# Kernel tuning notes

Hardware: AMD Instinct MI355X
Metric: run time of the kernel (lower is better)

Reference implementation:

```python
import jax, jax.numpy as jnp
import numpy as np

B, N, C = 4, 2048, 768
H = 12
HD = C // H
SCALE = HD ** -0.5


def setup_inputs() -> dict:
    key = jax.random.key(0)
    k1, k2, k3 = jax.random.split(key, 3)
    x = jax.random.normal(k1, (B, N, C), dtype=jnp.float32)
    w_qkv = jax.random.normal(k2, (3 * C, C), dtype=jnp.float32) * (C ** -0.5)
    w_proj = jax.random.normal(k3, (C, C), dtype=jnp.float32) * (C ** -0.5)
    b_proj = jnp.zeros((C,), dtype=jnp.float32)
    return {"x": x, "w_qkv": w_qkv, "w_proj": w_proj, "b_proj": b_proj}


def reference(x, w_qkv, w_proj, b_proj):
    Bx, Nx, Cx = x.shape
    # qkv linear: x @ W^T -> [B, N, 3C], then split into heads
    qkv = jnp.einsum('bnc,dc->bnd', x, w_qkv)
    qkv = qkv.reshape(Bx, Nx, 3, H, HD).transpose(2, 0, 3, 1, 4)  # [3, B, H, N, HD]
    q, k, v = qkv[0], qkv[1], qkv[2]
    attn = jnp.einsum('bhqd,bhkd->bhqk', q, k) * SCALE  # [B, H, N, N]
    attn = jax.nn.softmax(attn, axis=-1)
    out = jnp.einsum('bhqk,bhkd->bhqd', attn, v)  # [B, H, N, HD]
    out = out.transpose(0, 2, 1, 3).reshape(Bx, Nx, Cx)
    out = jnp.einsum('bnc,dc->bnd', out, w_proj) + b_proj
    return out
```

## Files before the change

### kernel.cpp

```cpp
#include <hip/hip_runtime.h>
#include <hip/hip_bf16.h>
#include <stdint.h>

#define DI __device__ __forceinline__

typedef __bf16 bf16x8 __attribute__((ext_vector_type(8)));
typedef float f32x4 __attribute__((ext_vector_type(4)));
typedef unsigned short u16;

DI u16 f2bf(float f) {
  union { float f; uint32_t u; } x; x.f = f;
  uint32_t r = (x.u + 0x7FFFu + ((x.u >> 16) & 1u)) >> 16;
  return (u16)r;
}
DI bf16x8 load16(const u16* p) { return *(const bf16x8*)p; }

DI void async_copy16(void* lds, const void* g) {
  __builtin_amdgcn_global_load_lds(
      (const __attribute__((address_space(1))) uint32_t*)g,
      (__attribute__((address_space(3))) uint32_t*)lds, 16, 0, 0);
}

DI f32x4 mfma16(bf16x8 a, bf16x8 b, f32x4 c) {
  return __builtin_amdgcn_mfma_f32_16x16x32_bf16(a, b, c, 0, 0, 0);
}

DI float redsum16(float v) {
  v += __shfl_xor(v, 1);
  v += __shfl_xor(v, 2);
  v += __shfl_xor(v, 4);
  v += __shfl_xor(v, 8);
  return v;
}

DI uint32_t pk_bf16(float a, float b) {
  union { __hip_bfloat162 v; uint32_t u; } r;
  r.v = __float22bfloat162_rn(make_float2(a, b));
  return r.u;
}

#define QSCALE (0.125f * 1.44269504088896340736f)

__global__ __launch_bounds__(256)
void cvt_all(const float* __restrict__ s0, u16* __restrict__ d0, int n0,
             const float* __restrict__ s1, u16* __restrict__ d1, int n1,
             const float* __restrict__ s2, u16* __restrict__ d2, int n2) {
  int i = (blockIdx.x * 256 + threadIdx.x) * 4;
  const float* s; u16* d;
  if (i < n0) { s = s0 + i; d = d0 + i; }
  else if (i < n0 + n1) { s = s1 + (i - n0); d = d1 + (i - n0); }
  else if (i < n0 + n1 + n2) { s = s2 + (i - n0 - n1); d = d2 + (i - n0 - n1); }
  else return;
  float4 v = *(const float4*)s;
  ushort4 o;
  o.x = f2bf(v.x); o.y = f2bf(v.y); o.z = f2bf(v.z); o.w = f2bf(v.w);
  *(ushort4*)d = o;
}

__global__ __launch_bounds__(256)
void gemm_qkv(const u16* __restrict__ A, const u16* __restrict__ Bm,
              u16* __restrict__ Qb, u16* __restrict__ Kb, u16* __restrict__ Vt,
              int M, int N, int K) {
  __shared__ u16 As[128 * 32];
  __shared__ u16 Bs[128 * 32];

  const int tid  = threadIdx.x;
  const int lane = tid & 63;
  const int wave = tid >> 6;
  const int m0 = blockIdx.y * 128;
  const int n0 = blockIdx.x * 128;
  const int wm = (wave & 1) * 64;
  const int wn = (wave >> 1) * 64;
  const int c = lane & 15;
  const int g = lane >> 4;

  f32x4 acc[4][4] = {};

  for (int k0 = 0; k0 < K; k0 += 32) {
#pragma unroll
    for (int i = 0; i < 2; ++i) {
      int j = i * 256 + tid;
      int row = j >> 2;
      int col = (j & 3) * 8;
      async_copy16(&As[j * 8], &A[(size_t)(m0 + row) * K + k0 + col]);
      async_copy16(&Bs[j * 8], &Bm[(size_t)(n0 + row) * K + k0 + col]);
    }
    __syncthreads();

    bf16x8 af[4], bfr[4];
#pragma unroll
    for (int t = 0; t < 4; ++t) {
      af[t]  = *(const bf16x8*)&As[(wm + t * 16 + c) * 32 + g * 8];
      bfr[t] = *(const bf16x8*)&Bs[(wn + t * 16 + c) * 32 + g * 8];
    }
#pragma unroll
    for (int mt = 0; mt < 4; ++mt)
#pragma unroll
      for (int nt = 0; nt < 4; ++nt)
        acc[mt][nt] = mfma16(af[mt], bfr[nt], acc[mt][nt]);
    __syncthreads();
  }

  if (n0 < 768) {
#pragma unroll
    for (int nt = 0; nt < 4; ++nt) {
      int col = n0 + wn + nt * 16 + c;
#pragma unroll
      for (int mt = 0; mt < 4; ++mt)
#pragma unroll
        for (int r = 0; r < 4; ++r) {
          int row = m0 + wm + mt * 16 + g * 4 + r;
          Qb[(size_t)row * 768 + col] = f2bf(acc[mt][nt][r] * QSCALE);
        }
    }
  } else if (n0 < 1536) {
#pragma unroll
    for (int nt = 0; nt < 4; ++nt) {
      int col = n0 - 768 + wn + nt * 16 + c;
#pragma unroll
      for (int mt = 0; mt < 4; ++mt)
#pragma unroll
        for (int r = 0; r < 4; ++r) {
          int row = m0 + wm + mt * 16 + g * 4 + r;
          Kb[(size_t)row * 768 + col] = f2bf(acc[mt][nt][r]);
        }
    }
  } else {
#pragma unroll
    for (int nt = 0; nt < 4; ++nt) {
      int cv = n0 - 1536 + wn + nt * 16 + c;
      int hv = cv >> 6, d = cv & 63;
#pragma unroll
      for (int mt = 0; mt < 4; ++mt) {
        int row = m0 + wm + mt * 16 + g * 4;
        int b = row >> 11, nn = row & 2047;
        ushort4 o;
        o.x = f2bf(acc[mt][nt][0]); o.y = f2bf(acc[mt][nt][1]);
        o.z = f2bf(acc[mt][nt][2]); o.w = f2bf(acc[mt][nt][3]);
        *(ushort4*)&Vt[(((size_t)b * 12 + hv) * 64 + d) * 2048 + nn] = o;
      }
    }
  }
}

__global__ __launch_bounds__(256)
void gemm_proj(const u16* __restrict__ A, const u16* __restrict__ Bm,
               const float* __restrict__ bias, float* __restrict__ Co,
               int M, int N, int K) {
  __shared__ u16 As[128 * 32];
  __shared__ u16 Bs[128 * 32];

  const int tid  = threadIdx.x;
  const int lane = tid & 63;
  const int wave = tid >> 6;
  const int m0 = blockIdx.y * 128;
  const int n0 = blockIdx.x * 128;
  const int wm = (wave & 1) * 64;
  const int wn = (wave >> 1) * 64;
  const int c = lane & 15;
  const int g = lane >> 4;

  f32x4 acc[4][4] = {};

  for (int k0 = 0; k0 < K; k0 += 32) {
#pragma unroll
    for (int i = 0; i < 2; ++i) {
      int j = i * 256 + tid;
      int row = j >> 2;
      int col = (j & 3) * 8;
      async_copy16(&As[j * 8], &A[(size_t)(m0 + row) * K + k0 + col]);
      async_copy16(&Bs[j * 8], &Bm[(size_t)(n0 + row) * K + k0 + col]);
    }
    __syncthreads();

    bf16x8 af[4], bfr[4];
#pragma unroll
    for (int t = 0; t < 4; ++t) {
      af[t]  = *(const bf16x8*)&As[(wm + t * 16 + c) * 32 + g * 8];
      bfr[t] = *(const bf16x8*)&Bs[(wn + t * 16 + c) * 32 + g * 8];
    }
#pragma unroll
    for (int mt = 0; mt < 4; ++mt)
#pragma unroll
      for (int nt = 0; nt < 4; ++nt)
        acc[mt][nt] = mfma16(af[mt], bfr[nt], acc[mt][nt]);
    __syncthreads();
  }

#pragma unroll
  for (int nt = 0; nt < 4; ++nt) {
    int col = n0 + wn + nt * 16 + c;
    float bv = bias[col];
#pragma unroll
    for (int mt = 0; mt < 4; ++mt)
#pragma unroll
      for (int r = 0; r < 4; ++r) {
        int row = m0 + wm + mt * 16 + g * 4 + r;
        Co[(size_t)row * N + col] = acc[mt][nt][r] + bv;
      }
  }
}

__global__ __launch_bounds__(256)
void attn_flash(const u16* __restrict__ Qb, const u16* __restrict__ Kb,
                const u16* __restrict__ Vt, u16* __restrict__ out) {
  __shared__ u16 Ks[2 * 64 * 32];
  __shared__ u16 Vs[2 * 64 * 32];
  __shared__ __align__(16) u16 Plds[4][32 * 72];

  const int tid  = threadIdx.x;
  const int lane = tid & 63;
  const int wave = tid >> 6;
  const int idx = blockIdx.x;
  const int qchunk = idx & 15;
  const int h = (idx >> 4) % 12;
  const int b = idx / (16 * 12);
  const int q0 = qchunk * 128 + wave * 32;
  const int c = lane & 15;
  const int g = lane >> 4;

  const u16* Qp = Qb + (size_t)b * 2048 * 768 + h * 64;
  const u16* Kp = Kb + (size_t)b * 2048 * 768 + h * 64;
  const u16* Vp = Vt + ((size_t)b * 12 + h) * 64 * 2048;

  u16* pw = &Plds[wave][0];

  const bf16x8 qf0 = load16(&Qp[(size_t)(q0 + c) * 768 + g * 8]);
  const bf16x8 qf1 = load16(&Qp[(size_t)(q0 + c) * 768 + 32 + g * 8]);
  const bf16x8 qg0 = load16(&Qp[(size_t)(q0 + 16 + c) * 768 + g * 8]);
  const bf16x8 qg1 = load16(&Qp[(size_t)(q0 + 16 + c) * 768 + 32 + g * 8]);

  const int j0 = tid, j1 = tid + 256;

  float lsum0[4] = {0.f, 0.f, 0.f, 0.f};
  float lsum1[4] = {0.f, 0.f, 0.f, 0.f};
  f32x4 o0[4] = {}, o1[4] = {};

  for (int k0 = 0; k0 < 2048; k0 += 64) {
    {
      int kk0 = (j0 >> 2) & 63, ch0 = j0 & 3;
      int kk1 = (j1 >> 2) & 63, ch1 = j1 & 3;
      async_copy16(&Ks[j0 * 8], &Kp[(size_t)(k0 + kk0) * 768 + ch0 * 8]);
      async_copy16(&Ks[j1 * 8], &Kp[(size_t)(k0 + kk1) * 768 + 32 + ch1 * 8]);
      async_copy16(&Vs[j0 * 8], &Vp[(size_t)kk0 * 2048 + k0 + ch0 * 8]);
      async_copy16(&Vs[j1 * 8], &Vp[(size_t)kk1 * 2048 + k0 + 32 + ch1 * 8]);
    }
    __syncthreads();

    f32x4 s0[4] = {}, s1[4] = {};
#pragma unroll
    for (int kt = 0; kt < 4; ++kt) {
      bf16x8 kf0 = *(const bf16x8*)&Ks[(kt * 16 + c) * 32 + g * 8];
      bf16x8 kf1 = *(const bf16x8*)&Ks[64 * 32 + (kt * 16 + c) * 32 + g * 8];
      s0[kt] = mfma16(qf0, kf0, s0[kt]);
      s0[kt] = mfma16(qf1, kf1, s0[kt]);
      s1[kt] = mfma16(qg0, kf0, s1[kt]);
      s1[kt] = mfma16(qg1, kf1, s1[kt]);
    }

#pragma unroll
    for (int kt = 0; kt < 4; ++kt) {
#pragma unroll
      for (int r2 = 0; r2 < 2; ++r2) {
        float pa = __builtin_amdgcn_exp2f(s0[kt][r2 * 2]);
        float pb = __builtin_amdgcn_exp2f(s0[kt][r2 * 2 + 1]);
        lsum0[r2 * 2] += pa; lsum0[r2 * 2 + 1] += pb;
        union { uint32_t u; u16 h[2]; } pk; pk.u = pk_bf16(pa, pb);
        pw[(g * 4 + r2 * 2) * 72 + kt * 16 + c]     = pk.h[0];
        pw[(g * 4 + r2 * 2 + 1) * 72 + kt * 16 + c] = pk.h[1];
        float qa = __builtin_amdgcn_exp2f(s1[kt][r2 * 2]);
        float qb = __builtin_amdgcn_exp2f(s1[kt][r2 * 2 + 1]);
        lsum1[r2 * 2] += qa; lsum1[r2 * 2 + 1] += qb;
        union { uint32_t u; u16 h[2]; } qk; qk.u = pk_bf16(qa, qb);
        pw[(16 + g * 4 + r2 * 2) * 72 + kt * 16 + c]     = qk.h[0];
        pw[(16 + g * 4 + r2 * 2 + 1) * 72 + kt * 16 + c] = qk.h[1];
      }
    }
    __asm__ volatile("s_waitcnt lgkmcnt(0)" ::: "memory");

#pragma unroll
    for (int kt2 = 0; kt2 < 2; ++kt2) {
      const bf16x8 pf0 = *(const bf16x8*)&pw[c * 72 + kt2 * 32 + g * 8];
      const bf16x8 pf1 = *(const bf16x8*)&pw[(16 + c) * 72 + kt2 * 32 + g * 8];
#pragma unroll
      for (int dt = 0; dt < 4; ++dt) {
        bf16x8 vf = *(const bf16x8*)&Vs[kt2 * 64 * 32 + (dt * 16 + c) * 32 + g * 8];
        o0[dt] = mfma16(pf0, vf, o0[dt]);
        o1[dt] = mfma16(pf1, vf, o1[dt]);
      }
    }
    __syncthreads();
  }

  float inv0[4], inv1[4];
#pragma unroll
  for (int r = 0; r < 4; ++r) {
    inv0[r] = 1.f / redsum16(lsum0[r]);
    inv1[r] = 1.f / redsum16(lsum1[r]);
  }
#pragma unroll
  for (int dt = 0; dt < 4; ++dt)
#pragma unroll
    for (int r = 0; r < 4; ++r) {
      int n = q0 + g * 4 + r;
      out[(size_t)(b * 2048 + n) * 768 + h * 64 + dt * 16 + c] =
          f2bf(o0[dt][r] * inv0[r]);
      out[(size_t)(b * 2048 + n + 16) * 768 + h * 64 + dt * 16 + c] =
          f2bf(o1[dt][r] * inv1[r]);
    }
}

extern "C" void kernel_launch(void* const* d_in, const int* in_sizes, int n_in,
                              void* d_out, int out_size, void* d_ws, size_t ws_size,
                              hipStream_t stream) {
  const float* x      = (const float*)d_in[0];
  const float* w_qkv  = (const float*)d_in[1];
  const float* w_proj = (const float*)d_in[2];
  const float* b_proj = (const float*)d_in[3];
  float* out = (float*)d_out;

  const int M = 8192;
  const int C = 768;
  const int NQKV = 2304;

  u16* xb     = (u16*)d_ws;
  u16* wqkvb  = xb + (size_t)M * C;
  u16* wprojb = wqkvb + (size_t)NQKV * C;
  u16* Qb     = wprojb + (size_t)C * C;
  u16* Kb     = Qb + (size_t)M * C;
  u16* Vt     = Kb + (size_t)M * C;
  u16* attn   = Vt + (size_t)M * C;

  dim3 blk(256);
  const int n0 = M * C, n1 = NQKV * C, n2 = C * C;
  cvt_all<<<dim3((n0 + n1 + n2) / 1024), blk, 0, stream>>>(
      x, xb, n0, w_qkv, wqkvb, n1, w_proj, wprojb, n2);

  gemm_qkv<<<dim3(NQKV / 128, M / 128), blk, 0, stream>>>(
      xb, wqkvb, Qb, Kb, Vt, M, NQKV, C);
  attn_flash<<<dim3(4 * 12 * 16), blk, 0, stream>>>(Qb, Kb, Vt, attn);
  gemm_proj<<<dim3(C / 128, M / 128), blk, 0, stream>>>(
      attn, wprojb, b_proj, out, M, C, C);
}
```

Baseline: 234.8 us.

## Transpose MFMA operands in attention and compute softmax row sums with MFMA

New measurement: 242.3 us. 3.2% more time.

```diff
diff --git a/kernel.cpp b/kernel.cpp
--- a/kernel.cpp
+++ b/kernel.cpp
@@ -23,14 +23,6 @@
 
 DI f32x4 mfma16(bf16x8 a, bf16x8 b, f32x4 c) {
   return __builtin_amdgcn_mfma_f32_16x16x32_bf16(a, b, c, 0, 0, 0);
-}
-
-DI float redsum16(float v) {
-  v += __shfl_xor(v, 1);
-  v += __shfl_xor(v, 2);
-  v += __shfl_xor(v, 4);
-  v += __shfl_xor(v, 8);
-  return v;
 }
 
 DI uint32_t pk_bf16(float a, float b) {
@@ -230,11 +222,14 @@
   const bf16x8 qg0 = load16(&Qp[(size_t)(q0 + 16 + c) * 768 + g * 8]);
   const bf16x8 qg1 = load16(&Qp[(size_t)(q0 + 16 + c) * 768 + 32 + g * 8]);
 
+  bf16x8 ones;
+#pragma unroll
+  for (int j = 0; j < 8; ++j) ones[j] = (__bf16)1.0f;
+
   const int j0 = tid, j1 = tid + 256;
 
-  float lsum0[4] = {0.f, 0.f, 0.f, 0.f};
-  float lsum1[4] = {0.f, 0.f, 0.f, 0.f};
   f32x4 o0[4] = {}, o1[4] = {};
+  f32x4 osum0 = {}, osum1 = {};
 
   for (int k0 = 0; k0 < 2048; k0 += 64) {
     {
@@ -247,34 +242,32 @@
     }
     __syncthreads();
 
-    f32x4 s0[4] = {}, s1[4] = {};
+    f32x4 st0[4], st1[4];
 #pragma unroll
     for (int kt = 0; kt < 4; ++kt) {
       bf16x8 kf0 = *(const bf16x8*)&Ks[(kt * 16 + c) * 32 + g * 8];
       bf16x8 kf1 = *(const bf16x8*)&Ks[64 * 32 + (kt * 16 + c) * 32 + g * 8];
-      s0[kt] = mfma16(qf0, kf0, s0[kt]);
-      s0[kt] = mfma16(qf1, kf1, s0[kt]);
-      s1[kt] = mfma16(qg0, kf0, s1[kt]);
-      s1[kt] = mfma16(qg1, kf1, s1[kt]);
+      f32x4 z = {};
+      st0[kt] = mfma16(kf0, qf0, z);
+      st0[kt] = mfma16(kf1, qf1, st0[kt]);
+      st1[kt] = mfma16(kf0, qg0, z);
+      st1[kt] = mfma16(kf1, qg1, st1[kt]);
     }
 
 #pragma unroll
     for (int kt = 0; kt < 4; ++kt) {
-#pragma unroll
-      for (int r2 = 0; r2 < 2; ++r2) {
-        float pa = __builtin_amdgcn_exp2f(s0[kt][r2 * 2]);
-        float pb = __builtin_amdgcn_exp2f(s0[kt][r2 * 2 + 1]);
-        lsum0[r2 * 2] += pa; lsum0[r2 * 2 + 1] += pb;
-        union { uint32_t u; u16 h[2]; } pk; pk.u = pk_bf16(pa, pb);
-        pw[(g * 4 + r2 * 2) * 72 + kt * 16 + c]     = pk.h[0];
-        pw[(g * 4 + r2 * 2 + 1) * 72 + kt * 16 + c] = pk.h[1];
-        float qa = __builtin_amdgcn_exp2f(s1[kt][r2 * 2]);
-        float qb = __builtin_amdgcn_exp2f(s1[kt][r2 * 2 + 1]);
-        lsum1[r2 * 2] += qa; lsum1[r2 * 2 + 1] += qb;
-        union { uint32_t u; u16 h[2]; } qk; qk.u = pk_bf16(qa, qb);
-        pw[(16 + g * 4 + r2 * 2) * 72 + kt * 16 + c]     = qk.h[0];
-        pw[(16 + g * 4 + r2 * 2 + 1) * 72 + kt * 16 + c] = qk.h[1];
-      }
+      float p0 = __builtin_amdgcn_exp2f(st0[kt][0]);
+      float p1 = __builtin_amdgcn_exp2f(st0[kt][1]);
+      float p2 = __builtin_amdgcn_exp2f(st0[kt][2]);
+      float p3 = __builtin_amdgcn_exp2f(st0[kt][3]);
+      *(uint2*)&pw[(size_t)c * 72 + kt * 16 + g * 4] =
+          make_uint2(pk_bf16(p0, p1), pk_bf16(p2, p3));
+      float q0v = __builtin_amdgcn_exp2f(st1[kt][0]);
+      float q1v = __builtin_amdgcn_exp2f(st1[kt][1]);
+      float q2v = __builtin_amdgcn_exp2f(st1[kt][2]);
+      float q3v = __builtin_amdgcn_exp2f(st1[kt][3]);
+      *(uint2*)&pw[(size_t)(16 + c) * 72 + kt * 16 + g * 4] =
+          make_uint2(pk_bf16(q0v, q1v), pk_bf16(q2v, q3v));
     }
     __asm__ volatile("s_waitcnt lgkmcnt(0)" ::: "memory");
 
@@ -285,29 +278,26 @@
 #pragma unroll
       for (int dt = 0; dt < 4; ++dt) {
         bf16x8 vf = *(const bf16x8*)&Vs[kt2 * 64 * 32 + (dt * 16 + c) * 32 + g * 8];
-        o0[dt] = mfma16(pf0, vf, o0[dt]);
-        o1[dt] = mfma16(pf1, vf, o1[dt]);
+        o0[dt] = mfma16(vf, pf0, o0[dt]);
+        o1[dt] = mfma16(vf, pf1, o1[dt]);
       }
-    }
-    __syncthreads();
-  }
-
-  float inv0[4], inv1[4];
-#pragma unroll
-  for (int r = 0; r < 4; ++r) {
-    inv0[r] = 1.f / redsum16(lsum0[r]);
-    inv1[r] = 1.f / redsum16(lsum1[r]);
-  }
-#pragma unroll
-  for (int dt = 0; dt < 4; ++dt)
-#pragma unroll
-    for (int r = 0; r < 4; ++r) {
-      int n = q0 + g * 4 + r;
-      out[(size_t)(b * 2048 + n) * 768 + h * 64 + dt * 16 + c] =
-          f2bf(o0[dt][r] * inv0[r]);
-      out[(size_t)(b * 2048 + n + 16) * 768 + h * 64 + dt * 16 + c] =
-          f2bf(o1[dt][r] * inv1[r]);
-    }
+      osum0 = mfma16(ones, pf0, osum0);
+      osum1 = mfma16(ones, pf1, osum1);
+    }
+    __syncthreads();
+  }
+
+  const float inv0 = 1.f / osum0[0];
+  const float inv1 = 1.f / osum1[0];
+#pragma unroll
+  for (int dt = 0; dt < 4; ++dt) {
+    uint2 w0 = make_uint2(pk_bf16(o0[dt][0] * inv0, o0[dt][1] * inv0),
+                          pk_bf16(o0[dt][2] * inv0, o0[dt][3] * inv0));
+    *(uint2*)&out[(size_t)(b * 2048 + q0 + c) * 768 + h * 64 + dt * 16 + g * 4] = w0;
+    uint2 w1 = make_uint2(pk_bf16(o1[dt][0] * inv1, o1[dt][1] * inv1),
+                          pk_bf16(o1[dt][2] * inv1, o1[dt][3] * inv1));
+    *(uint2*)&out[(size_t)(b * 2048 + q0 + 16 + c) * 768 + h * 64 + dt * 16 + g * 4] = w1;
+  }
 }
 
 extern "C" void kernel_launch(void* const* d_in, const int* in_sizes, int n_in,
```
